# Kernel optimization log

Measured on AMD Instinct MI355X. Metric: run time of the kernel, lower is better.

The kernel has to match this reference:

```python
import jax, jax.numpy as jnp
import numpy as np

TEMP = 1.0
EPS = 1e-15

B, N, F, K = 8, 2000, 128, 64


def setup_inputs() -> dict:
    key = jax.random.key(0)
    k1, k2, k3 = jax.random.split(key, 3)
    x = jax.random.normal(k1, (B, N, F), dtype=jnp.float32)
    adj = jax.random.uniform(k2, (B, N, N), dtype=jnp.float32)
    s = jax.random.normal(k3, (B, N, K), dtype=jnp.float32)
    mask = jnp.ones((B, N), dtype=bool)
    return {"x": x, "adj": adj, "s": s, "mask": mask}


def reference(x, adj, s, mask):
    k = s.shape[-1]
    s = jax.nn.softmax(s / TEMP, axis=-1)
    m = mask[..., None].astype(x.dtype)          # [B,N,1]
    x = x * m
    s = s * m

    # pooled features: s^T x -> [B,K,F]
    out = jnp.einsum('bnk,bnf->bkf', s, x)

    # pooled adjacency: s^T A s -> [B,K,K]
    as_ = jnp.einsum('bnm,bmk->bnk', adj, s)     # A s, [B,N,K]
    out_adj = jnp.einsum('bnk,bnl->bkl', as_, s)

    # mincut loss
    mincut_num = jnp.einsum('bkk->b', out_adj)
    d_flat = jnp.sum(adj, axis=-1)               # degree, [B,N]
    # trace(s^T diag(d) s) = sum_n d_n * sum_k s_nk^2 (avoids dense diag)
    mincut_den = jnp.einsum('bn,bnk,bnk->b', d_flat, s, s)
    mincut_loss = jnp.mean(-(mincut_num / mincut_den))

    # orthogonality loss
    ss = jnp.einsum('bnk,bnl->bkl', s, s)        # [B,K,K]
    ss_norm = jnp.linalg.norm(ss, axis=(-2, -1), keepdims=True)
    i_s = jnp.eye(k, dtype=ss.dtype)
    ortho = jnp.linalg.norm(ss / ss_norm - i_s / jnp.sqrt(jnp.asarray(k, ss.dtype)), axis=(-2, -1))
    ortho_loss = jnp.mean(ortho)

    # zero diagonal, symmetric degree normalization
    ind = jnp.arange(k)
    out_adj = out_adj.at[:, ind, ind].set(0.0)
    d = jnp.sqrt(jnp.sum(out_adj, axis=-1))[:, None, :] + EPS  # [B,1,K]
    out_adj = out_adj / d / jnp.swapaxes(d, 1, 2)

    return out, out_adj, mincut_loss, ortho_loss
```

## Files before the change

### kernel.cpp

```cpp
#include <hip/hip_runtime.h>

typedef __bf16 bf16;
typedef __bf16 bf16x4 __attribute__((ext_vector_type(4)));
typedef __bf16 bf16x8 __attribute__((ext_vector_type(8)));
typedef float f32x4 __attribute__((ext_vector_type(4)));

#define NB 8
#define NN 2000
#define N2 2048
#define KK 64
#define FF 128

__global__ __launch_bounds__(256) void k1_softmax(const float* __restrict__ s,
                                                  bf16* __restrict__ sT,
                                                  float* __restrict__ rowsq) {
  const int b = blockIdx.x >> 5, tile = blockIdx.x & 31;
  const int n0 = tile * 64;
  const int t = threadIdx.x;
  const int r = t >> 2, q = t & 3;
  __shared__ float ptile[64][65];
  const int n = n0 + r;
  const bool valid = n < NN;
  float v[16];
  if (valid) {
    const float4* src = (const float4*)(s + ((size_t)(b * NN + n)) * KK + q * 16);
#pragma unroll
    for (int i = 0; i < 4; ++i) {
      float4 f = src[i];
      v[4 * i + 0] = f.x; v[4 * i + 1] = f.y; v[4 * i + 2] = f.z; v[4 * i + 3] = f.w;
    }
  } else {
#pragma unroll
    for (int i = 0; i < 16; ++i) v[i] = 0.f;
  }
  float mx = v[0];
#pragma unroll
  for (int i = 1; i < 16; ++i) mx = fmaxf(mx, v[i]);
  mx = fmaxf(mx, __shfl_xor(mx, 1));
  mx = fmaxf(mx, __shfl_xor(mx, 2));
  float sum = 0.f;
#pragma unroll
  for (int i = 0; i < 16; ++i) { v[i] = __expf(v[i] - mx); sum += v[i]; }
  sum += __shfl_xor(sum, 1);
  sum += __shfl_xor(sum, 2);
  const float scale = valid ? (1.0f / sum) : 0.f;
  float rq = 0.f;
#pragma unroll
  for (int i = 0; i < 16; ++i) { v[i] *= scale; rq += v[i] * v[i]; }
  rq += __shfl_xor(rq, 1);
  rq += __shfl_xor(rq, 2);
  if (q == 0) rowsq[b * N2 + n0 + r] = rq;
#pragma unroll
  for (int i = 0; i < 16; ++i) ptile[r][q * 16 + i] = v[i];
  __syncthreads();
  bf16x8 o0, o1;
#pragma unroll
  for (int i = 0; i < 8; ++i) o0[i] = (bf16)ptile[q * 16 + i][r];
#pragma unroll
  for (int i = 0; i < 8; ++i) o1[i] = (bf16)ptile[q * 16 + 8 + i][r];
  bf16* dst = sT + ((size_t)(b * KK + r)) * N2 + n0 + q * 16;
  *(bf16x8*)dst = o0;
  *(bf16x8*)(dst + 8) = o1;
}

__global__ __launch_bounds__(512, 6) void k2_big(const float* __restrict__ adj,
                                                 const bf16* __restrict__ sT,
                                                 const float* __restrict__ x,
                                                 bf16* __restrict__ xT,
                                                 bf16* __restrict__ asT,
                                                 const float* __restrict__ rowsq,
                                                 float* __restrict__ den_part) {
  __shared__ __align__(16) char smem[52224];
  __shared__ float dredS[8];
  const int bid0 = blockIdx.x;
  const int t = threadIdx.x;

  if (bid0 >= 512) {
    const int q = bid0 - 512;
    const int bb = q & 7, tl = q >> 3;
    const int n0b = tl * 64;
    float* xt = (float*)smem;
#pragma unroll
    for (int i = 0; i < 4; ++i) {
      int idx = t + 512 * i;
      int row = idx >> 5, c4 = idx & 31;
      int n = n0b + row;
      float4 vv = make_float4(0.f, 0.f, 0.f, 0.f);
      if (n < NN) vv = ((const float4*)(x + ((size_t)(bb * NN + n)) * FF))[c4];
      *(float4*)&xt[row * 132 + c4 * 4] = vv;
    }
    __syncthreads();
    const int f = t >> 2, h = t & 3;
    bf16x8 o0, o1;
#pragma unroll
    for (int i = 0; i < 8; ++i) o0[i] = (bf16)xt[(h * 16 + i) * 132 + f];
#pragma unroll
    for (int i = 0; i < 8; ++i) o1[i] = (bf16)xt[(h * 16 + 8 + i) * 132 + f];
    bf16* dst = xT + ((size_t)(bb * FF + f)) * N2 + n0b + h * 16;
    *(bf16x8*)dst = o0;
    *(bf16x8*)(dst + 8) = o1;
    return;
  }

  const int b = bid0 & 7, tile = bid0 >> 3;
  const int n0 = tile * 32;

  const int w = t >> 6, l = t & 63;
  const int lr = l & 15, lg = l >> 4;
  const int nr = w & 1, kr = w >> 1;

  const int srow = t >> 4, scp = t & 15;
  const int brow = t >> 3, bcol = t & 7;
  const bool avalid = (n0 + srow) < NN;
  const float4* arowp = (const float4*)(adj +
      ((size_t)(b * NN) + (avalid ? (n0 + srow) : 0)) * NN);
  const bf16* sTrp = sT + ((size_t)(b * KK + brow)) * N2;

  const int afo = (nr * 16 + lr) * 136;
  const int bfo = 4352 + (kr * 16 + lr) * 136;

  f32x4 acc;
#pragma unroll
  for (int r = 0; r < 4; ++r) acc[r] = 0.f;

  float4 La0, La1;
  bf16x8 Lb0, Lb1;

#define K2_LOAD(C)                                                          \
  {                                                                         \
    const int base_ = (C) * 32 + scp * 2;                                   \
    const int i0_ = base_ > 499 ? 499 : base_;                              \
    const int i1_ = base_ + 1 > 499 ? 499 : base_ + 1;                      \
    if (avalid) { La0 = arowp[i0_]; La1 = arowp[i1_]; }                     \
    else { La0 = make_float4(0.f,0.f,0.f,0.f); La1 = La0; }                 \
    Lb0 = *(const bf16x8*)(sTrp + (C) * 128 + bcol * 8);                    \
    Lb1 = *(const bf16x8*)(sTrp + (C) * 128 + 64 + bcol * 8);               \
  }

#define K2_WRITE(BUF)                                                      \
  {                                                                        \
    bf16x8 av_;                                                            \
    av_[0] = (bf16)La0.x; av_[1] = (bf16)La0.y;                            \
    av_[2] = (bf16)La0.z; av_[3] = (bf16)La0.w;                            \
    av_[4] = (bf16)La1.x; av_[5] = (bf16)La1.y;                            \
    av_[6] = (bf16)La1.z; av_[7] = (bf16)La1.w;                            \
    bf16* bb_ = (bf16*)smem + (BUF) * 13056;                               \
    *(bf16x8*)(bb_ + srow * 136 + scp * 8) = av_;                          \
    *(bf16x8*)(bb_ + 4352 + brow * 136 + bcol * 8) = Lb0;                  \
    *(bf16x8*)(bb_ + 4352 + brow * 136 + 64 + bcol * 8) = Lb1;             \
  }

#define K2_MFMA(BUF)                                                        \
  {                                                                         \
    const bf16* base_ = (bf16*)smem + (BUF) * 13056;                        \
    _Pragma("unroll")                                                       \
    for (int ms = 0; ms < 4; ++ms) {                                        \
      bf16x8 af_ = *(const bf16x8*)(base_ + afo + ms * 32 + lg * 8);        \
      bf16x8 bf_ = *(const bf16x8*)(base_ + bfo + ms * 32 + lg * 8);        \
      acc = __builtin_amdgcn_mfma_f32_16x16x32_bf16(af_, bf_, acc, 0, 0, 0);\
    }                                                                       \
  }

  K2_LOAD(0);
  K2_WRITE(0);
  __syncthreads();
  for (int c = 0; c < 16; ++c) {
    if (c < 15) K2_LOAD(c + 1);
    K2_MFMA(c & 1);
    if (c < 15) K2_WRITE((c + 1) & 1);
    __syncthreads();
  }
#undef K2_LOAD
#undef K2_WRITE
#undef K2_MFMA

  bf16x4 o;
#pragma unroll
  for (int r = 0; r < 4; ++r) o[r] = (bf16)acc[r];
  *(bf16x4*)(asT + ((size_t)(b * KK + kr * 16 + lr)) * N2 + n0 + nr * 16 + lg * 4) = o;

  float s0 = acc[0], s1 = acc[1], s2 = acc[2], s3 = acc[3];
#pragma unroll
  for (int off = 1; off <= 8; off <<= 1) {
    s0 += __shfl_xor(s0, off); s1 += __shfl_xor(s1, off);
    s2 += __shfl_xor(s2, off); s3 += __shfl_xor(s3, off);
  }
  const float* rqp = rowsq + b * N2 + n0 + nr * 16 + lg * 4;
  float part = s0 * rqp[0] + s1 * rqp[1] + s2 * rqp[2] + s3 * rqp[3];
  part += __shfl_xor(part, 16);
  part += __shfl_xor(part, 32);
  if (l == 0) dredS[w] = part;
  __syncthreads();
  if (t == 0) {
    float dt = 0.f;
#pragma unroll
    for (int i = 0; i < 8; ++i) dt += dredS[i];
    den_part[b * 64 + tile] = dt;
  }
}

__global__ __launch_bounds__(256) void k3_gemms(const bf16* __restrict__ sT,
                                                const bf16* __restrict__ asT,
                                                const bf16* __restrict__ xT,
                                                float* __restrict__ adjraw,
                                                float* __restrict__ ssw,
                                                float* __restrict__ dout) {
  const int lgc = (blockIdx.x & 7) * 64 + (blockIdx.x >> 3);
  const int b = lgc >> 6, u = lgc & 63;
  const bf16 *Ab, *Bb;
  float* Cb;
  int ldC;
  if (u < 16) {
    const int rt = u >> 2, ct = u & 3;
    Ab = asT + ((size_t)(b * KK + rt * 16)) * N2;
    Bb = sT + ((size_t)(b * KK + ct * 16)) * N2;
    Cb = adjraw + b * KK * KK + rt * 16 * KK + ct * 16; ldC = KK;
  } else if (u < 32) {
    const int v = u - 16, rt = v >> 2, ct = v & 3;
    Ab = sT + ((size_t)(b * KK + rt * 16)) * N2;
    Bb = sT + ((size_t)(b * KK + ct * 16)) * N2;
    Cb = ssw + b * KK * KK + rt * 16 * KK + ct * 16; ldC = KK;
  } else {
    const int v = u - 32, rt = v >> 3, ct = v & 7;
    Ab = sT + ((size_t)(b * KK + rt * 16)) * N2;
    Bb = xT + ((size_t)(b * FF + ct * 16)) * N2;
    Cb = dout + b * KK * FF + rt * 16 * FF + ct * 16; ldC = FF;
  }
  const int t = threadIdx.x;
  const int w = t >> 6, l = t & 63;
  const int lr = l & 15, lg = l >> 4;
  f32x4 acc;
#pragma unroll
  for (int r = 0; r < 4; ++r) acc[r] = 0.f;
  const int m_begin = w * 512;
#pragma unroll 4
  for (int s = 0; s < 16; ++s) {
    const int m = m_begin + s * 32 + lg * 8;
    bf16x8 af = *(const bf16x8*)(Ab + (size_t)lr * N2 + m);
    bf16x8 bfv = *(const bf16x8*)(Bb + (size_t)lr * N2 + m);
    acc = __builtin_amdgcn_mfma_f32_16x16x32_bf16(af, bfv, acc, 0, 0, 0);
  }
  __shared__ float red[4][16][16];
#pragma unroll
  for (int r = 0; r < 4; ++r) red[w][lg * 4 + r][lr] = acc[r];
  __syncthreads();
  const int row = t >> 4, col = t & 15;
  const float v = red[0][row][col] + red[1][row][col] +
                  red[2][row][col] + red[3][row][col];
  Cb[row * ldC + col] = v;
}

__device__ inline float wred64(float v) {
#pragma unroll
  for (int off = 32; off > 0; off >>= 1) v += __shfl_xor(v, off);
  return v;
}

__global__ __launch_bounds__(512) void k4_final(const float* __restrict__ adjraw,
                                                const float* __restrict__ ssw,
                                                const float* __restrict__ den_part,
                                                float* __restrict__ dout) {
  const int b = threadIdx.x >> 6;
  const int lane = threadIdx.x & 63;
  const float den = wred64(den_part[b * 64 + lane]);
  const float* arow = adjraw + b * 4096 + lane * 64;
  float4 av[16];
#pragma unroll
  for (int i = 0; i < 16; ++i) av[i] = ((const float4*)arow)[i];
  const float diag = adjraw[b * 4096 + lane * 65];
  float rs = 0.f;
#pragma unroll
  for (int i = 0; i < 16; ++i) rs += av[i].x + av[i].y + av[i].z + av[i].w;
  rs -= diag;
  rs = fmaxf(rs, 0.f);
  const float num = wred64(diag);
  const float d = sqrtf(rs) + 1e-15f;
  __shared__ float dsh[8][64];
  __shared__ float lossm[8], losso[8];
  dsh[b][lane] = d;
  __syncthreads();
  const float invd = 1.0f / d;
  float* orow = dout + NB * KK * FF + b * 4096 + lane * 64;
#pragma unroll
  for (int i = 0; i < 16; ++i) {
    float4 cvv = av[i];
    cvv.x = (4 * i + 0 == lane) ? 0.f : cvv.x * invd / dsh[b][4 * i + 0];
    cvv.y = (4 * i + 1 == lane) ? 0.f : cvv.y * invd / dsh[b][4 * i + 1];
    cvv.z = (4 * i + 2 == lane) ? 0.f : cvv.z * invd / dsh[b][4 * i + 2];
    cvv.w = (4 * i + 3 == lane) ? 0.f : cvv.w * invd / dsh[b][4 * i + 3];
    ((float4*)orow)[i] = cvv;
  }
  const float* srow = ssw + b * 4096 + lane * 64;
  float4 sv[16];
  float sq = 0.f;
#pragma unroll
  for (int i = 0; i < 16; ++i) {
    sv[i] = ((const float4*)srow)[i];
    sq += sv[i].x * sv[i].x + sv[i].y * sv[i].y + sv[i].z * sv[i].z + sv[i].w * sv[i].w;
  }
  const float frob = sqrtf(wred64(sq));
  const float fi = 1.0f / frob;
  float osum = 0.f;
#pragma unroll
  for (int i = 0; i < 16; ++i) {
    float tx = sv[i].x * fi - ((4 * i + 0 == lane) ? 0.125f : 0.f);
    float ty = sv[i].y * fi - ((4 * i + 1 == lane) ? 0.125f : 0.f);
    float tz = sv[i].z * fi - ((4 * i + 2 == lane) ? 0.125f : 0.f);
    float tw = sv[i].w * fi - ((4 * i + 3 == lane) ? 0.125f : 0.f);
    osum += tx * tx + ty * ty + tz * tz + tw * tw;
  }
  const float ot = wred64(osum);
  if (lane == 0) {
    lossm[b] = -(num / den);
    losso[b] = sqrtf(ot);
  }
  __syncthreads();
  if (threadIdx.x == 0) {
    float m = 0.f, oo = 0.f;
#pragma unroll
    for (int b2 = 0; b2 < 8; ++b2) { m += lossm[b2]; oo += losso[b2]; }
    dout[NB * KK * FF + NB * KK * KK + 0] = m * 0.125f;
    dout[NB * KK * FF + NB * KK * KK + 1] = oo * 0.125f;
  }
}

extern "C" void kernel_launch(void* const* d_in, const int* in_sizes, int n_in,
                              void* d_out, int out_size, void* d_ws, size_t ws_size,
                              hipStream_t stream) {
  const float* x = (const float*)d_in[0];
  const float* adj = (const float*)d_in[1];
  const float* s = (const float*)d_in[2];
  float* out = (float*)d_out;
  char* ws = (char*)d_ws;
  bf16* sT = (bf16*)ws;
  bf16* xT = (bf16*)(ws + (2u << 20));
  bf16* asT = (bf16*)(ws + (6u << 20));
  float* rowsq = (float*)(ws + (8u << 20));
  float* den_part = (float*)(ws + (8u << 20) + 65536);
  float* adjraw = (float*)(ws + (8u << 20) + 65536 + 4096);
  float* ssw = adjraw + NB * KK * KK;

  k1_softmax<<<256, 256, 0, stream>>>(s, sT, rowsq);
  k2_big<<<768, 512, 0, stream>>>(adj, sT, x, xT, asT, rowsq, den_part);
  k3_gemms<<<512, 256, 0, stream>>>(sT, asT, xT, adjraw, ssw, out);
  k4_final<<<1, 512, 0, stream>>>(adjraw, ssw, den_part, out);
}
```

Before: 230.5 us.

## Stream adjacency and sT tiles into LDS via async global_load_lds pipeline

Replaces the register-staged, double-buffered load/convert/store loop in the A·s GEMM kernel with direct global-to-LDS loads into four LDS stages, ordered by vmcnt waits and barriers. Adjacency is now kept as fp32 in LDS with an XOR-swizzled layout and converted to bf16 just before each MFMA. The change aims to cut VGPR staging and the LDS write instructions, and to keep more memory traffic in flight across the 32 smaller chunks. In exchange, the last chunk reads past column 2000 of each row with no clamp, relying on zero-padded sT to cancel those terms, and could read past the end of the buffer on the final row.

```diff
diff --git a/kernel.cpp b/kernel.cpp
--- a/kernel.cpp
+++ b/kernel.cpp
@@ -63,14 +63,14 @@
   *(bf16x8*)(dst + 8) = o1;
 }
 
-__global__ __launch_bounds__(512, 6) void k2_big(const float* __restrict__ adj,
-                                                 const bf16* __restrict__ sT,
-                                                 const float* __restrict__ x,
-                                                 bf16* __restrict__ xT,
-                                                 bf16* __restrict__ asT,
-                                                 const float* __restrict__ rowsq,
-                                                 float* __restrict__ den_part) {
-  __shared__ __align__(16) char smem[52224];
+__global__ __launch_bounds__(512) void k2_dma(const float* __restrict__ adj,
+                                              const bf16* __restrict__ sT,
+                                              const float* __restrict__ x,
+                                              bf16* __restrict__ xT,
+                                              bf16* __restrict__ asT,
+                                              const float* __restrict__ rowsq,
+                                              float* __restrict__ den_part) {
+  __shared__ __align__(16) float smemf[16384];
   __shared__ float dredS[8];
   const int bid0 = blockIdx.x;
   const int t = threadIdx.x;
@@ -79,7 +79,7 @@
     const int q = bid0 - 512;
     const int bb = q & 7, tl = q >> 3;
     const int n0b = tl * 64;
-    float* xt = (float*)smem;
+    float* xt = smemf;
 #pragma unroll
     for (int i = 0; i < 4; ++i) {
       int idx = t + 512 * i;
@@ -109,69 +109,70 @@
   const int lr = l & 15, lg = l >> 4;
   const int nr = w & 1, kr = w >> 1;
 
-  const int srow = t >> 4, scp = t & 15;
-  const int brow = t >> 3, bcol = t & 7;
-  const bool avalid = (n0 + srow) < NN;
-  const float4* arowp = (const float4*)(adj +
-      ((size_t)(b * NN) + (avalid ? (n0 + srow) : 0)) * NN);
-  const bf16* sTrp = sT + ((size_t)(b * KK + brow)) * N2;
-
-  const int afo = (nr * 16 + lr) * 136;
-  const int bfo = 4352 + (kr * 16 + lr) * 136;
+  const int arow_l = (w << 2) + (l >> 4);
+  int an = n0 + arow_l; if (an > NN - 1) an = NN - 1;
+  const int aslot = (l & 15) ^ ((arow_l & 7) << 1);
+  const float* aSrc = adj + ((size_t)(b * NN) + an) * NN + aslot * 4;
+  const int brow_l = (w << 3) + (l >> 3);
+  const int bslot = (l & 7) ^ (brow_l & 7);
+  const bf16* bSrc = sT + ((size_t)(b * KK) + brow_l) * N2 + bslot * 8;
 
   f32x4 acc;
 #pragma unroll
   for (int r = 0; r < 4; ++r) acc[r] = 0.f;
 
-  float4 La0, La1;
-  bf16x8 Lb0, Lb1;
-
-#define K2_LOAD(C)                                                          \
-  {                                                                         \
-    const int base_ = (C) * 32 + scp * 2;                                   \
-    const int i0_ = base_ > 499 ? 499 : base_;                              \
-    const int i1_ = base_ + 1 > 499 ? 499 : base_ + 1;                      \
-    if (avalid) { La0 = arowp[i0_]; La1 = arowp[i1_]; }                     \
-    else { La0 = make_float4(0.f,0.f,0.f,0.f); La1 = La0; }                 \
-    Lb0 = *(const bf16x8*)(sTrp + (C) * 128 + bcol * 8);                    \
-    Lb1 = *(const bf16x8*)(sTrp + (C) * 128 + 64 + bcol * 8);               \
-  }
-
-#define K2_WRITE(BUF)                                                      \
-  {                                                                        \
-    bf16x8 av_;                                                            \
-    av_[0] = (bf16)La0.x; av_[1] = (bf16)La0.y;                            \
-    av_[2] = (bf16)La0.z; av_[3] = (bf16)La0.w;                            \
-    av_[4] = (bf16)La1.x; av_[5] = (bf16)La1.y;                            \
-    av_[6] = (bf16)La1.z; av_[7] = (bf16)La1.w;                            \
-    bf16* bb_ = (bf16*)smem + (BUF) * 13056;                               \
-    *(bf16x8*)(bb_ + srow * 136 + scp * 8) = av_;                          \
-    *(bf16x8*)(bb_ + 4352 + brow * 136 + bcol * 8) = Lb0;                  \
-    *(bf16x8*)(bb_ + 4352 + brow * 136 + 64 + bcol * 8) = Lb1;             \
-  }
-
-#define K2_MFMA(BUF)                                                        \
-  {                                                                         \
-    const bf16* base_ = (bf16*)smem + (BUF) * 13056;                        \
-    _Pragma("unroll")                                                       \
-    for (int ms = 0; ms < 4; ++ms) {                                        \
-      bf16x8 af_ = *(const bf16x8*)(base_ + afo + ms * 32 + lg * 8);        \
-      bf16x8 bf_ = *(const bf16x8*)(base_ + bfo + ms * 32 + lg * 8);        \
-      acc = __builtin_amdgcn_mfma_f32_16x16x32_bf16(af_, bf_, acc, 0, 0, 0);\
-    }                                                                       \
-  }
-
-  K2_LOAD(0);
-  K2_WRITE(0);
-  __syncthreads();
-  for (int c = 0; c < 16; ++c) {
-    if (c < 15) K2_LOAD(c + 1);
-    K2_MFMA(c & 1);
-    if (c < 15) K2_WRITE((c + 1) & 1);
-    __syncthreads();
-  }
-#undef K2_LOAD
-#undef K2_WRITE
+#define K2_ISSUE(C, BUF)                                                       \
+  do {                                                                         \
+    __builtin_amdgcn_global_load_lds(aSrc + (size_t)(C) * 64,                  \
+                                     smemf + (BUF) * 4096 + (w << 8), 16, 0, 0);\
+    __builtin_amdgcn_global_load_lds(bSrc + (C) * 64,                          \
+                                     smemf + (BUF) * 4096 + 2048 + (w << 8),   \
+                                     16, 0, 0);                                \
+  } while (0)
+
+#define K2_MFMA(BUF)                                                           \
+  do {                                                                         \
+    const float* Ab_ = smemf + (BUF) * 4096 + (nr * 16 + lr) * 64;             \
+    const bf16* Bb_ = (const bf16*)(smemf + (BUF) * 4096 + 2048) +             \
+                      (kr * 16 + lr) * 64;                                     \
+    _Pragma("unroll")                                                          \
+    for (int ks = 0; ks < 2; ++ks) {                                           \
+      const int sA = ((ks * 8 + lg * 2) ^ ((lr & 7) << 1)) * 4;                \
+      f32x4 a0 = *(const f32x4*)(Ab_ + sA);                                    \
+      f32x4 a1 = *(const f32x4*)(Ab_ + sA + 4);                                \
+      bf16x8 af;                                                               \
+      af[0] = (bf16)a0[0]; af[1] = (bf16)a0[1];                                \
+      af[2] = (bf16)a0[2]; af[3] = (bf16)a0[3];                                \
+      af[4] = (bf16)a1[0]; af[5] = (bf16)a1[1];                                \
+      af[6] = (bf16)a1[2]; af[7] = (bf16)a1[3];                                \
+      bf16x8 bf_ = *(const bf16x8*)(Bb_ + (((ks * 4 + lg) ^ (lr & 7)) << 3));  \
+      acc = __builtin_amdgcn_mfma_f32_16x16x32_bf16(af, bf_, acc, 0, 0, 0);    \
+    }                                                                          \
+  } while (0)
+
+  K2_ISSUE(0, 0);
+  K2_ISSUE(1, 1);
+  K2_ISSUE(2, 2);
+  for (int c = 0; c < 29; ++c) {
+    asm volatile("s_waitcnt vmcnt(4)" ::: "memory");
+    __builtin_amdgcn_s_barrier();
+    asm volatile("" ::: "memory");
+    K2_ISSUE(c + 3, (c + 3) & 3);
+    K2_MFMA(c & 3);
+  }
+  asm volatile("s_waitcnt vmcnt(4)" ::: "memory");
+  __builtin_amdgcn_s_barrier();
+  asm volatile("" ::: "memory");
+  K2_MFMA(1);
+  asm volatile("s_waitcnt vmcnt(2)" ::: "memory");
+  __builtin_amdgcn_s_barrier();
+  asm volatile("" ::: "memory");
+  K2_MFMA(2);
+  asm volatile("s_waitcnt vmcnt(0)" ::: "memory");
+  __builtin_amdgcn_s_barrier();
+  asm volatile("" ::: "memory");
+  K2_MFMA(3);
+#undef K2_ISSUE
 #undef K2_MFMA
 
   bf16x4 o;
@@ -341,7 +342,7 @@
   float* ssw = adjraw + NB * KK * KK;
 
   k1_softmax<<<256, 256, 0, stream>>>(s, sT, rowsq);
-  k2_big<<<768, 512, 0, stream>>>(adj, sT, x, xT, asT, rowsq, den_part);
+  k2_dma<<<768, 512, 0, stream>>>(adj, sT, x, xT, asT, rowsq, den_part);
   k3_gemms<<<512, 256, 0, stream>>>(sT, asT, xT, adjraw, ssw, out);
   k4_final<<<1, 512, 0, stream>>>(adjraw, ssw, den_part, out);
 }
```

After: 233.7 us. No clear change (+1.4%).
